# Kernel tuning notes

Hardware: AMD Instinct MI355X
Metric: run time of the kernel (lower is better)

Reference implementation:

```python
import jax, jax.numpy as jnp
import numpy as np

S = 2          # scale_int = ceil(scale)
K = 3          # kernel size
OUTC = 3       # num_out_ch
NUM_FEAT = 64


def conv3x3(x, w, b):
    y = jax.lax.conv_general_dilated(x, w, (1, 1), ((1, 1), (1, 1)),
                                     dimension_numbers=('NCHW', 'OIHW', 'NCHW'))
    return y + b[None, :, None, None]


def unfold3x3(x):
    # torch F.unfold(x, 3, padding=1): (N, C*9, H*W), order c*9 + ki*3 + kj
    N, C, H, W = x.shape
    xp = jnp.pad(x, ((0, 0), (0, 0), (1, 1), (1, 1)))
    patches = jnp.stack([xp[:, :, i:i + H, j:j + W]
                         for i in range(3) for j in range(3)], axis=2)  # (N,C,9,H,W)
    return patches.reshape(N, C * 9, H * W)


def setup_inputs() -> dict:
    key = jax.random.key(0)
    ks = jax.random.split(key, 12)
    b, t, c, h, w = 2, 4, 16, 64, 64
    H, W = S * h, S * w
    nf4 = 64 // 4  # 16
    d_w = K * K * NUM_FEAT * OUTC  # 1728
    return {
        'x0': jax.random.normal(ks[0], (b, NUM_FEAT, h, w), jnp.float32),
        'feature': jax.random.normal(ks[1], (b, t, c, h, w), jnp.float32),
        'pos_mat': jax.random.uniform(ks[2], (H, W, 3), jnp.float32),
        'mask': jnp.ones((b, OUTC, H, W), dtype=bool),
        'conv1_w': jax.random.normal(ks[3], (nf4, 64, 3, 3), jnp.float32) * 0.05,
        'conv1_b': jnp.zeros((nf4,), jnp.float32),
        'conv2_w': jax.random.normal(ks[4], (nf4, nf4, 3, 3), jnp.float32) * 0.05,
        'conv2_b': jnp.zeros((nf4,), jnp.float32),
        'f2w1_w': jax.random.normal(ks[5], (256, nf4 + 1), jnp.float32) * 0.05,
        'f2w1_b': jnp.zeros((256,), jnp.float32),
        'f2w2_w': jax.random.normal(ks[6], (d_w, 256), jnp.float32) * 0.05,
        'f2w2_b': jnp.zeros((d_w,), jnp.float32),
    }


def reference(x0, feature, pos_mat, mask, conv1_w, conv1_b, conv2_w, conv2_b,
              f2w1_w, f2w1_b, f2w2_w, f2w2_b):
    b, t, c, h, w = feature.shape
    H, W = S * h, S * w
    # with_gradBack=False -> feature.detach()
    feat = jax.lax.stop_gradient(feature).reshape(b, t * c, h, w)
    # repeat_x(..., upsample=True): nearest-neighbour upsample by S
    feat_up = jnp.repeat(jnp.repeat(feat, S, axis=2), S, axis=3)  # (b,64,H,W)
    f = jax.nn.relu(conv3x3(feat_up, conv1_w, conv1_b))
    f = conv3x3(f, conv2_w, conv2_b)                              # (b,16,H,W)
    pos0 = jnp.transpose(pos_mat, (2, 0, 1))[0:1]                 # (1,H,W)
    fm = jnp.concatenate([f, jnp.broadcast_to(pos0[None], (b, 1, H, W))], axis=1)
    fm = fm.reshape(b, -1, H * W).transpose(0, 2, 1)              # (b,HW,17)
    hdn = jax.nn.relu(fm @ f2w1_w.T + f2w1_b)
    weights = hdn @ f2w2_w.T + f2w2_b                             # (b,HW,1728)
    weights = weights.reshape(b, h, S, w, S, K * K * NUM_FEAT, OUTC)
    weights = jnp.transpose(weights, (0, 2, 4, 1, 3, 5, 6))
    weights = weights.reshape(b, S * S, h * w, K * K * NUM_FEAT, OUTC)
    # repeat_x(x0) tiles x0 S^2 times -> all S^2 col copies identical; compute once
    cols = unfold3x3(x0).transpose(0, 2, 1)                       # (b,hw,576)
    out = jnp.einsum('bpk,bspko->bspo', cols, weights)            # (b,S^2,hw,3)
    out = jnp.transpose(out, (0, 1, 3, 2)).reshape(b, S, S, OUTC, h, w)
    out = jnp.transpose(out, (0, 3, 4, 1, 5, 2)).reshape(b, OUTC, H, W)
    # integer scale -> mask all True -> masked_select + view is identity
    return out, weights
```

## Files before the change

### kernel.cpp

```cpp
#include <hip/hip_runtime.h>

#define THREADS 256

#define Bsz 2
#define HWp 16384
#define Ntot (Bsz*HWp)
#define HID 256
#define Mm 1728
#define FMC 17
#define W_OFF 98304

#define F1_OFF  0
#define F1_SZ   (Bsz*16*HWp)
#define WB2_OFF (F1_SZ + Ntot*FMC)
#define WB1_OFF (WB2_OFF + (Mm*HID)/2)

typedef __attribute__((ext_vector_type(8))) short bf16x8;
typedef __attribute__((ext_vector_type(4))) float f32x4;

static __device__ __forceinline__ short f2bf(float x) {
    unsigned u = __builtin_bit_cast(unsigned, x);
    unsigned r = (u + 0x7fff + ((u >> 16) & 1)) >> 16;
    return (short)r;
}
static __device__ __forceinline__ float bf2f(short s) {
    unsigned u = ((unsigned)(unsigned short)s) << 16;
    return __builtin_bit_cast(float, u);
}

__global__ __launch_bounds__(THREADS) void k13_conv1_cvt(const float* __restrict__ feat,
                                                         const float* __restrict__ w1,
                                                         const float* __restrict__ b1,
                                                         float* __restrict__ f1,
                                                         const float* __restrict__ w2g,
                                                         short* __restrict__ wB2,
                                                         const float* __restrict__ w1g,
                                                         short* __restrict__ wB1) {
    int tid = threadIdx.x;
    if (blockIdx.x >= 944) {
        for (int idx = tid; idx < 8192; idx += THREADS) {
            int i = idx & 7, l = (idx >> 3) & 63, h = idx >> 9;
            int k = (l >> 4) * 8 + i, hid = h * 16 + (l & 15);
            wB1[idx] = (k < FMC) ? f2bf(w1g[hid * FMC + k]) : (short)0;
        }
        return;
    }
    if (blockIdx.x >= 512) {
        int t4 = ((blockIdx.x - 512) * THREADS + tid) * 4;
        int i = t4 & 7, l = (t4 >> 3) & 63, ct = (t4 >> 9) & 3, s = (t4 >> 11) & 7, mc = t4 >> 14;
        int col = mc * 64 + ct * 16 + (l & 15);
        int k0 = s * 32 + (l >> 4) * 8 + i;
        f32x4 w = *(const f32x4*)(w2g + col * HID + k0);
        short4 o;
        o.x = f2bf(w[0]); o.y = f2bf(w[1]); o.z = f2bf(w[2]); o.w = f2bf(w[3]);
        *(short4*)(wB2 + t4) = o;
        return;
    }
    __shared__ float sW[4 * 64 * 4];
    int b = blockIdx.x;
    int rg = b & 15, oc = (b >> 4) & 15, bb = b >> 8;
    int c = tid & 63, r = rg * 4 + (tid >> 6);

    #pragma unroll
    for (int q = 0; q < 4; ++q) {
        int e = tid * 4 + q;
        int v = e & 1, u = (e >> 1) & 1, ic = (e >> 2) & 63, pp = (e >> 8) & 3;
        int pi = pp >> 1, pj = pp & 1;
        float s = 0.f;
        for (int ki = 0; ki < 3; ++ki) {
            bool okki = pi ? (u ? (ki == 2) : (ki <= 1)) : (u ? (ki >= 1) : (ki == 0));
            if (!okki) continue;
            for (int kj = 0; kj < 3; ++kj) {
                bool okkj = pj ? (v ? (kj == 2) : (kj <= 1)) : (v ? (kj >= 1) : (kj == 0));
                if (okkj) s += w1[((oc * 64 + ic) * 3 + ki) * 3 + kj];
            }
        }
        sW[(pp * 64 + ic) * 4 + u * 2 + v] = s;
    }
    __syncthreads();

    float bias = b1[oc];
    float a00 = bias, a01 = bias, a10 = bias, a11 = bias;

    float mt = (r > 0) ? 1.f : 0.f, mb2 = (r < 63) ? 1.f : 0.f;
    float ml = (c > 0) ? 1.f : 0.f, mr2 = (c < 63) ? 1.f : 0.f;
    int ro0 = (r > 0) ? -64 : 0, ro2 = (r < 63) ? 64 : 0;
    int co0 = (c > 0) ? -1 : 0, co2 = (c < 63) ? 1 : 0;

    const float* fb = feat + bb * 64 * 4096 + r * 64 + c;
    for (int ic = 0; ic < 64; ++ic) {
        const float* p1 = fb + ic * 4096;
        const float* p0 = p1 + ro0;
        const float* p2 = p1 + ro2;
        float v00 = p0[co0] * (mt * ml), v01 = p0[0] * mt, v02 = p0[co2] * (mt * mr2);
        float v10 = p1[co0] * ml,        v11 = p1[0],      v12 = p1[co2] * mr2;
        float v20 = p2[co0] * (mb2 * ml), v21 = p2[0] * mb2, v22 = p2[co2] * (mb2 * mr2);

        f32x4 w0 = *(const f32x4*)(sW + (0 * 64 + ic) * 4);
        f32x4 w1v = *(const f32x4*)(sW + (1 * 64 + ic) * 4);
        f32x4 w2v = *(const f32x4*)(sW + (2 * 64 + ic) * 4);
        f32x4 w3 = *(const f32x4*)(sW + (3 * 64 + ic) * 4);

        a00 = fmaf(w0[0], v00, a00); a00 = fmaf(w0[1], v01, a00);
        a00 = fmaf(w0[2], v10, a00); a00 = fmaf(w0[3], v11, a00);
        a01 = fmaf(w1v[0], v01, a01); a01 = fmaf(w1v[1], v02, a01);
        a01 = fmaf(w1v[2], v11, a01); a01 = fmaf(w1v[3], v12, a01);
        a10 = fmaf(w2v[0], v10, a10); a10 = fmaf(w2v[1], v11, a10);
        a10 = fmaf(w2v[2], v20, a10); a10 = fmaf(w2v[3], v21, a10);
        a11 = fmaf(w3[0], v11, a11); a11 = fmaf(w3[1], v12, a11);
        a11 = fmaf(w3[2], v21, a11); a11 = fmaf(w3[3], v22, a11);
    }

    float* fo = f1 + (bb * 16 + oc) * HWp + (2 * r) * 128 + 2 * c;
    *reinterpret_cast<float2*>(fo)       = make_float2(fmaxf(a00, 0.f), fmaxf(a01, 0.f));
    *reinterpret_cast<float2*>(fo + 128) = make_float2(fmaxf(a10, 0.f), fmaxf(a11, 0.f));
}

__global__ __launch_bounds__(THREADS, 2) void k4_fused(const float* __restrict__ f1,
                                                       const float* __restrict__ w2,
                                                       const float* __restrict__ b2,
                                                       const float* __restrict__ pos,
                                                       const short* __restrict__ wB1,
                                                       const float* __restrict__ b1g,
                                                       const short* __restrict__ wB2,
                                                       const float* __restrict__ b2g,
                                                       const float* __restrict__ x0g,
                                                       float* __restrict__ dout) {
    __shared__ short sA[16384];
    __shared__ int   sOB[64];
    __shared__ float uni[3696];
    __shared__ short sStage[16384];

    short* sF  = (short*)uni;
    float* sFM = uni + 1584;
    short* sXT = (short*)uni;

    int tid = threadIdx.x;
    int n0 = blockIdx.x * 64;
    int bb = n0 >> 14, tt = n0 & 16383, I = tt >> 7, J0 = tt & 127;
    int i0 = I >> 1, jmin = J0 >> 1;

    for (int e = tid; e < 3168; e += THREADS) {
        int jc = e % 66, r2 = e / 66;
        int di = r2 % 3, ic = r2 / 3;
        int y = I + di - 1, x = J0 + jc - 1;
        float v = 0.f;
        if ((unsigned)y < 128u && (unsigned)x < 128u)
            v = f1[(bb * 16 + ic) * HWp + y * 128 + x];
        sF[(ic * 3 + di) * 66 + jc] = f2bf(v);
    }
    for (int e = tid; e < 2112; e += THREADS) sFM[e] = 0.f;
    if (tid < 64) {
        int J = J0 + tid;
        int s = ((I & 1) << 1) | (J & 1);
        int p = ((I >> 1) << 6) | (J >> 1);
        sOB[tid] = W_OFF + ((bb * 4 + s) * 4096 + p) * Mm;
    }
    __syncthreads();

    {
        int pix = tid & 63, q = tid >> 6;
        float acc[4];
        #pragma unroll
        for (int o = 0; o < 4; ++o) acc[o] = b2[q * 4 + o];
        #pragma unroll 4
        for (int ic = 0; ic < 16; ++ic) {
            float v[9];
            #pragma unroll
            for (int di = 0; di < 3; ++di) {
                const short* row = sF + (ic * 3 + di) * 66 + pix;
                v[di * 3 + 0] = bf2f(row[0]);
                v[di * 3 + 1] = bf2f(row[1]);
                v[di * 3 + 2] = bf2f(row[2]);
            }
            #pragma unroll
            for (int o = 0; o < 4; ++o) {
                const float* w = w2 + ((q * 4 + o) * 16 + ic) * 9;
                acc[o] = fmaf(v[0], w[0], acc[o]); acc[o] = fmaf(v[1], w[1], acc[o]);
                acc[o] = fmaf(v[2], w[2], acc[o]); acc[o] = fmaf(v[3], w[3], acc[o]);
                acc[o] = fmaf(v[4], w[4], acc[o]); acc[o] = fmaf(v[5], w[5], acc[o]);
                acc[o] = fmaf(v[6], w[6], acc[o]); acc[o] = fmaf(v[7], w[7], acc[o]);
                acc[o] = fmaf(v[8], w[8], acc[o]);
            }
        }
        #pragma unroll
        for (int o = 0; o < 4; ++o) sFM[pix * 33 + q * 4 + o] = acc[o];
        if (q == 0) sFM[pix * 33 + 16] = pos[(I * 128 + J0 + pix) * 3];
    }
    __syncthreads();

    int wv = tid >> 6, l = tid & 63, lm = l & 15, lg = l >> 4;

    int row = wv * 16 + lm;
    bf16x8 af1;
    #pragma unroll
    for (int i = 0; i < 8; ++i) af1[i] = f2bf(sFM[row * 33 + lg * 8 + i]);
    __syncthreads();

    {
        const short* wb = wB1 + l * 8;
        int pbase = ((lg >> 1) * 64 + row) * 8 + (lg & 1) * 4;
        #pragma unroll 4
        for (int h = 0; h < 16; ++h) {
            bf16x8 bfr = *(const bf16x8*)(wb + h * 512);
            f32x4 bias = *(const f32x4*)(b1g + h * 16 + lg * 4);
            f32x4 acc = __builtin_amdgcn_mfma_f32_16x16x32_bf16(bfr, af1, bias, 0, 0, 0);
            unsigned c0 = (unsigned short)f2bf(fmaxf(acc[0], 0.f));
            unsigned c1 = (unsigned short)f2bf(fmaxf(acc[1], 0.f));
            unsigned c2 = (unsigned short)f2bf(fmaxf(acc[2], 0.f));
            unsigned c3 = (unsigned short)f2bf(fmaxf(acc[3], 0.f));
            uint2 uv; uv.x = c0 | (c1 << 16); uv.y = c2 | (c3 << 16);
            *(uint2*)(sA + pbase + h * 1024) = uv;
        }
    }
    {
        const float* x0b = x0g + bb * 64 * 4096;
        for (int e = tid; e < 6528; e += THREADS) {
            int ch = e / 102, r2 = e - ch * 102;
            int ki = r2 / 34, jc = r2 - ki * 34;
            int y = i0 + ki - 1, x = jmin + jc - 1;
            float v = 0.f;
            if ((unsigned)y < 64u && (unsigned)x < 64u) v = x0b[(ch * 64 + y) * 64 + x];
            sXT[jc * 195 + ch * 3 + ki] = f2bf(v);
        }
    }
    __syncthreads();

    int lg3 = lg % 3, lg4 = lg * 4;
    int jl195[4];
    #pragma unroll
    for (int rt = 0; rt < 4; ++rt)
        jl195[rt] = (rt * 8 + (lm >> 1)) * 195;

    int sOBr[16];
    #pragma unroll
    for (int g = 0; g < 16; ++g) sOBr[g] = sOB[g * 4 + lg];

    const short* aptr = sA + lg * 512 + lm * 8;
    short* myStage = sStage + wv * 4096;

    float racc[4][3];
    #pragma unroll
    for (int rt = 0; rt < 4; ++rt) {
        racc[rt][0] = 0.f; racc[rt][1] = 0.f; racc[rt][2] = 0.f;
    }

#define ACCUM(QB)                                                              \
        _Pragma("unroll")                                                      \
        for (int ct = 0; ct < 4; ++ct) {                                       \
            int t = m0 + ct * 16 + lg4;                                        \
            int K0 = (t * 21846) >> 16;                                        \
            int rem3 = t - 3 * K0;                                             \
            int Q2 = (K0 * 21846) >> 16;                                       \
            int kja = K0 - 3 * Q2;                                             \
            int kqa = kja * 195 + Q2;                                          \
            int kqb = (kja == 2) ? (Q2 + 1) : (kqa + 195);                     \
            _Pragma("unroll")                                                  \
            for (int rt = 0; rt < 4; ++rt) {                                   \
                float xa = bf2f(sXT[jl195[rt] + kqa]);                         \
                float xb = bf2f(sXT[jl195[rt] + kqb]);                         \
                float x1 = (rem3 == 2) ? xb : xa;                              \
                float x2 = (rem3 >= 1) ? xb : xa;                              \
                racc[rt][(QB + ct) % 3] =                                      \
                    fmaf(acc[rt][ct][0], xa, racc[rt][(QB + ct) % 3]);         \
                racc[rt][(QB + ct + 1) % 3] =                                  \
                    fmaf(acc[rt][ct][1], x1, racc[rt][(QB + ct + 1) % 3]);     \
                racc[rt][(QB + ct + 2) % 3] =                                  \
                    fmaf(acc[rt][ct][2], x2, racc[rt][(QB + ct + 2) % 3]);     \
                racc[rt][(QB + ct) % 3] =                                      \
                    fmaf(acc[rt][ct][3], xb, racc[rt][(QB + ct) % 3]);         \
            }                                                                  \
        }

    int lo = (wv < 3) ? wv * 7 : 21;
    int hi = (wv < 3) ? (lo + 7) : 27;
    for (int mc = lo; mc < hi; ++mc) {
        int m0 = mc * 64;
        f32x4 acc[4][4];
        #pragma unroll
        for (int ct = 0; ct < 4; ++ct) {
            f32x4 bias4 = *(const f32x4*)(b2g + m0 + ct * 16 + lg4);
            #pragma unroll
            for (int rt = 0; rt < 4; ++rt)
                acc[rt][ct] = bias4;
        }
        const short* bbase = wB2 + (size_t)mc * 16384 + l * 8;
        #pragma unroll 2
        for (int s = 0; s < 8; ++s) {
            bf16x8 af[4], bfr[4];
            #pragma unroll
            for (int rt = 0; rt < 4; ++rt)
                af[rt] = *(const bf16x8*)(aptr + s * 2048 + rt * 128);
            #pragma unroll
            for (int ct = 0; ct < 4; ++ct)
                bfr[ct] = *(const bf16x8*)(bbase + (s * 4 + ct) * 512);
            #pragma unroll
            for (int rt = 0; rt < 4; ++rt)
                #pragma unroll
                for (int ct = 0; ct < 4; ++ct)
                    acc[rt][ct] = __builtin_amdgcn_mfma_f32_16x16x32_bf16(
                        bfr[ct], af[rt], acc[rt][ct], 0, 0, 0);
        }
        #pragma unroll
        for (int rt = 0; rt < 4; ++rt) {
            int pxb = (rt * 16 + lm) * 64;
            #pragma unroll
            for (int ct = 0; ct < 4; ++ct) {
                int up = (((ct * 4 + lg) ^ lm) << 2);
                short4 sv;
                sv.x = f2bf(acc[rt][ct][0]); sv.y = f2bf(acc[rt][ct][1]);
                sv.z = f2bf(acc[rt][ct][2]); sv.w = f2bf(acc[rt][ct][3]);
                *(short4*)(myStage + pxb + up) = sv;
            }
        }
        switch (mc % 3) {
            case 0: ACCUM(0); break;
            case 1: ACCUM(1); break;
            default: ACCUM(2); break;
        }
        #pragma unroll
        for (int g = 0; g < 16; ++g) {
            int px = g * 4 + lg;
            int up = ((lm ^ (px & 15)) << 2);
            uint2 uv = *(const uint2*)(myStage + px * 64 + up);
            f32x4 v;
            v[0] = __builtin_bit_cast(float, uv.x << 16);
            v[1] = __builtin_bit_cast(float, uv.x & 0xffff0000u);
            v[2] = __builtin_bit_cast(float, uv.y << 16);
            v[3] = __builtin_bit_cast(float, uv.y & 0xffff0000u);
            *(f32x4*)(dout + sOBr[g] + m0 + lm * 4) = v;
        }
    }
#undef ACCUM

    __syncthreads();
    float* sOut = (float*)sStage;

    #pragma unroll
    for (int rt = 0; rt < 4; ++rt) {
        float q0 = racc[rt][0], q1 = racc[rt][1], q2 = racc[rt][2];
        float a0 = (lg3 == 0) ? q0 : ((lg3 == 1) ? q2 : q1);
        float a1 = (lg3 == 0) ? q1 : ((lg3 == 1) ? q0 : q2);
        float a2 = (lg3 == 0) ? q2 : ((lg3 == 1) ? q1 : q0);
        a0 += __shfl_xor(a0, 16, 64); a0 += __shfl_xor(a0, 32, 64);
        a1 += __shfl_xor(a1, 16, 64); a1 += __shfl_xor(a1, 32, 64);
        a2 += __shfl_xor(a2, 16, 64); a2 += __shfl_xor(a2, 32, 64);
        if (l < 16) {
            float* so = sOut + (wv * 64 + rt * 16 + lm) * 3;
            so[0] = a0; so[1] = a1; so[2] = a2;
        }
    }
    __syncthreads();
    if (tid < 192) {
        float s = sOut[tid] + sOut[192 + tid] + sOut[384 + tid] + sOut[576 + tid];
        int pix = tid / 3, o = tid - 3 * pix;
        dout[bb * 3 * HWp + o * HWp + I * 128 + J0 + pix] = s;
    }
}

extern "C" void kernel_launch(void* const* d_in, const int* in_sizes, int n_in,
                              void* d_out, int out_size, void* d_ws, size_t ws_size,
                              hipStream_t stream) {
    const float* x0      = (const float*)d_in[0];
    const float* feature = (const float*)d_in[1];
    const float* pos     = (const float*)d_in[2];
    const float* w1      = (const float*)d_in[4];
    const float* b1      = (const float*)d_in[5];
    const float* w2      = (const float*)d_in[6];
    const float* b2      = (const float*)d_in[7];
    const float* f2w1_w  = (const float*)d_in[8];
    const float* f2w1_b  = (const float*)d_in[9];
    const float* f2w2_w  = (const float*)d_in[10];
    const float* f2w2_b  = (const float*)d_in[11];

    float* out = (float*)d_out;
    float* ws  = (float*)d_ws;
    float* f1  = ws + F1_OFF;
    short* wB2 = (short*)(ws + WB2_OFF);
    short* wB1 = (short*)(ws + WB1_OFF);

    k13_conv1_cvt<<<945, THREADS, 0, stream>>>(feature, w1, b1, f1, f2w2_w, wB2,
                                               f2w1_w, wB1);
    k4_fused<<<Ntot / 64, THREADS, 0, stream>>>(f1, w2, b2, pos, wB1, f2w1_b,
                                                wB2, f2w2_b, x0, out);
}
```

Measured before the change: 106.3 us.

## Split waves by pixel half and column half, hoist A fragments into registers

Work is now split across the four waves as two pixel halves times two column-chunk halves (14 and 13 chunks), where before each wave covered all 64 pixels for a quarter of the chunks. Each wave keeps its 32-pixel A operand in registers for the whole loop instead of reloading it from LDS every step, and the staging buffer and reduction shrink to match. Each B tile loaded from global memory now feeds only 2 row tiles rather than 4, so B traffic per block doubles. The 16 bf16x8 A fragments held in registers may also raise register pressure.

```diff
diff --git a/kernel.cpp b/kernel.cpp
--- a/kernel.cpp
+++ b/kernel.cpp
@@ -129,7 +129,7 @@
     __shared__ short sA[16384];
     __shared__ int   sOB[64];
     __shared__ float uni[3696];
-    __shared__ short sStage[16384];
+    __shared__ short sStage[8192];
 
     short* sF  = (short*)uni;
     float* sFM = uni + 1584;
@@ -227,21 +227,31 @@
     __syncthreads();
 
     int lg3 = lg % 3, lg4 = lg * 4;
-    int jl195[4];
-    #pragma unroll
-    for (int rt = 0; rt < 4; ++rt)
-        jl195[rt] = (rt * 8 + (lm >> 1)) * 195;
-
-    int sOBr[16];
-    #pragma unroll
-    for (int g = 0; g < 16; ++g) sOBr[g] = sOB[g * 4 + lg];
-
-    const short* aptr = sA + lg * 512 + lm * 8;
-    short* myStage = sStage + wv * 4096;
-
-    float racc[4][3];
-    #pragma unroll
-    for (int rt = 0; rt < 4; ++rt) {
+    int h = wv & 1;
+    int chh = wv >> 1;
+
+    int jl195[2];
+    #pragma unroll
+    for (int rt = 0; rt < 2; ++rt)
+        jl195[rt] = (h * 16 + rt * 8 + (lm >> 1)) * 195;
+
+    int sOBr[8];
+    #pragma unroll
+    for (int g = 0; g < 8; ++g) sOBr[g] = sOB[h * 32 + g * 4 + lg];
+
+    const short* abase = sA + lg * 512 + h * 256 + lm * 8;
+    bf16x8 af[2][8];
+    #pragma unroll
+    for (int rt = 0; rt < 2; ++rt)
+        #pragma unroll
+        for (int s = 0; s < 8; ++s)
+            af[rt][s] = *(const bf16x8*)(abase + s * 2048 + rt * 128);
+
+    short* myStage = sStage + wv * 2048;
+
+    float racc[2][3];
+    #pragma unroll
+    for (int rt = 0; rt < 2; ++rt) {
         racc[rt][0] = 0.f; racc[rt][1] = 0.f; racc[rt][2] = 0.f;
     }
 
@@ -256,7 +266,7 @@
             int kqa = kja * 195 + Q2;                                          \
             int kqb = (kja == 2) ? (Q2 + 1) : (kqa + 195);                     \
             _Pragma("unroll")                                                  \
-            for (int rt = 0; rt < 4; ++rt) {                                   \
+            for (int rt = 0; rt < 2; ++rt) {                                   \
                 float xa = bf2f(sXT[jl195[rt] + kqa]);                         \
                 float xb = bf2f(sXT[jl195[rt] + kqb]);                         \
                 float x1 = (rem3 == 2) ? xb : xa;                              \
@@ -272,37 +282,33 @@
             }                                                                  \
         }
 
-    int lo = (wv < 3) ? wv * 7 : 21;
-    int hi = (wv < 3) ? (lo + 7) : 27;
+    int lo = chh ? 14 : 0;
+    int hi = chh ? 27 : 14;
     for (int mc = lo; mc < hi; ++mc) {
         int m0 = mc * 64;
-        f32x4 acc[4][4];
+        f32x4 acc[2][4];
         #pragma unroll
         for (int ct = 0; ct < 4; ++ct) {
             f32x4 bias4 = *(const f32x4*)(b2g + m0 + ct * 16 + lg4);
-            #pragma unroll
-            for (int rt = 0; rt < 4; ++rt)
-                acc[rt][ct] = bias4;
+            acc[0][ct] = bias4;
+            acc[1][ct] = bias4;
         }
         const short* bbase = wB2 + (size_t)mc * 16384 + l * 8;
-        #pragma unroll 2
+        #pragma unroll
         for (int s = 0; s < 8; ++s) {
-            bf16x8 af[4], bfr[4];
-            #pragma unroll
-            for (int rt = 0; rt < 4; ++rt)
-                af[rt] = *(const bf16x8*)(aptr + s * 2048 + rt * 128);
+            bf16x8 bfr[4];
             #pragma unroll
             for (int ct = 0; ct < 4; ++ct)
                 bfr[ct] = *(const bf16x8*)(bbase + (s * 4 + ct) * 512);
             #pragma unroll
-            for (int rt = 0; rt < 4; ++rt)
+            for (int rt = 0; rt < 2; ++rt)
                 #pragma unroll
                 for (int ct = 0; ct < 4; ++ct)
                     acc[rt][ct] = __builtin_amdgcn_mfma_f32_16x16x32_bf16(
-                        bfr[ct], af[rt], acc[rt][ct], 0, 0, 0);
-        }
-        #pragma unroll
-        for (int rt = 0; rt < 4; ++rt) {
+                        bfr[ct], af[rt][s], acc[rt][ct], 0, 0, 0);
+        }
+        #pragma unroll
+        for (int rt = 0; rt < 2; ++rt) {
             int pxb = (rt * 16 + lm) * 64;
             #pragma unroll
             for (int ct = 0; ct < 4; ++ct) {
@@ -319,10 +325,10 @@
             default: ACCUM(2); break;
         }
         #pragma unroll
-        for (int g = 0; g < 16; ++g) {
-            int px = g * 4 + lg;
-            int up = ((lm ^ (px & 15)) << 2);
-            uint2 uv = *(const uint2*)(myStage + px * 64 + up);
+        for (int g = 0; g < 8; ++g) {
+            int pxl = g * 4 + lg;
+            int up = ((lm ^ (pxl & 15)) << 2);
+            uint2 uv = *(const uint2*)(myStage + pxl * 64 + up);
             f32x4 v;
             v[0] = __builtin_bit_cast(float, uv.x << 16);
             v[1] = __builtin_bit_cast(float, uv.x & 0xffff0000u);
@@ -337,7 +343,7 @@
     float* sOut = (float*)sStage;
 
     #pragma unroll
-    for (int rt = 0; rt < 4; ++rt) {
+    for (int rt = 0; rt < 2; ++rt) {
         float q0 = racc[rt][0], q1 = racc[rt][1], q2 = racc[rt][2];
         float a0 = (lg3 == 0) ? q0 : ((lg3 == 1) ? q2 : q1);
         float a1 = (lg3 == 0) ? q1 : ((lg3 == 1) ? q0 : q2);
@@ -346,14 +352,15 @@
         a1 += __shfl_xor(a1, 16, 64); a1 += __shfl_xor(a1, 32, 64);
         a2 += __shfl_xor(a2, 16, 64); a2 += __shfl_xor(a2, 32, 64);
         if (l < 16) {
-            float* so = sOut + (wv * 64 + rt * 16 + lm) * 3;
+            float* so = sOut + (wv * 32 + rt * 16 + lm) * 3;
             so[0] = a0; so[1] = a1; so[2] = a2;
         }
     }
     __syncthreads();
     if (tid < 192) {
-        float s = sOut[tid] + sOut[192 + tid] + sOut[384 + tid] + sOut[576 + tid];
         int pix = tid / 3, o = tid - 3 * pix;
+        int hh = pix >> 5, pl = pix & 31;
+        float s = sOut[(hh * 32 + pl) * 3 + o] + sOut[((hh + 2) * 32 + pl) * 3 + o];
         dout[bb * 3 * HWp + o * HWp + I * 128 + J0 + pix] = s;
     }
 }
```

Result: no change. 108.3 us (+1.9%).
